# Performance work log

Hardware: AMD Instinct MI355X
Metric: run time of the kernel (lower is better)

## Reference

```python
import jax, jax.numpy as jnp
import numpy as np


def setup_inputs() -> dict:
    key = jax.random.key(0)
    k1, k2, k3, k4 = jax.random.split(key, 4)
    B, Cin, Cout, K, Wd, H, Wsp = 16, 256, 256, 3, 256, 64, 64
    fan_in = Cin * K * K
    return {
        "x": jax.random.normal(k1, (B, Cin, H, Wsp), dtype=jnp.float32),
        "w": jax.random.normal(k2, (B, Wd), dtype=jnp.float32),
        "conv_weight": jax.random.normal(k3, (Cout, Cin, K, K), dtype=jnp.float32) * 0.05,
        "style_w": jax.random.normal(k4, (Cin, Wd), dtype=jnp.float32) * 0.05,
        "style_b": jnp.zeros((Cin,), dtype=jnp.float32),
        "scale": jnp.asarray(1.0 / np.sqrt(fan_in), dtype=jnp.float32),
    }


def reference(x, w, conv_weight, style_w, style_b, scale):
    # x: [B, Cin, H, W]; w: [B, Wd]; conv_weight: [Cout, Cin, K, K]
    B, Cin, H, Wsp = x.shape
    Cout, _, K, _ = conv_weight.shape
    # style modulation: s = Linear(w) -> [B, 1, Cin, 1, 1]
    s = (w @ style_w.T + style_b).reshape(B, 1, Cin, 1, 1)
    # modulate + demodulate per-sample weights: [B, Cout, Cin, K, K]
    wt = (conv_weight * scale)[None] * s
    demod = jax.lax.rsqrt(jnp.sum(wt * wt, axis=(2, 3, 4), keepdims=True) + 1e-8)
    wt = (wt * demod).reshape(B * Cout, Cin, K, K)
    # grouped conv emulation: input [1, B*Cin, H, W], groups=B
    xr = x.reshape(1, B * Cin, H, Wsp)
    pad = 1
    out = jax.lax.conv_general_dilated(
        xr, wt,
        window_strides=(1, 1),
        padding=[(pad, pad), (pad, pad)],
        dimension_numbers=("NCHW", "OIHW", "NCHW"),
        feature_group_count=B,
    )
    return out.reshape(B, Cout, out.shape[2], out.shape[3])
```

## Files before the change

kernel.cpp:

```cpp
#include <hip/hip_runtime.h>
#include <hip/hip_bf16.h>

#define BB   16
#define CIN  256
#define COUT 256
#define WD   256
#define HH   64
#define WWS  64
#define NSP  4096
#define KW   9

typedef __attribute__((ext_vector_type(8))) short short8;
typedef __attribute__((ext_vector_type(4))) float f32x4;
typedef unsigned short ushort_t;
typedef unsigned int uint_t;

#define S_BYTES (BB*CIN*4)
#define WT_OFF (S_BYTES)
#define WT_BYTES (BB*9*COUT*CIN*2)
#define X_OFF (WT_OFF + WT_BYTES)
#define X_BYTES (BB*NSP*CIN*2)
#define ZP_OFF (X_OFF + X_BYTES)
#define ZP_BYTES 4096
#define WS_NEEDED ((size_t)(ZP_OFF + ZP_BYTES))

#define WAITVM0 asm volatile("s_waitcnt vmcnt(0)" ::: "memory")
#define WAITVM3 asm volatile("s_waitcnt vmcnt(3)" ::: "memory")

__device__ inline ushort_t f2bf(float f) {
    __hip_bfloat16 h = __float2bfloat16(f);
    return __builtin_bit_cast(ushort_t, h);
}

__device__ inline void gload_lds16(const ushort_t* g, ushort_t* l) {
    __builtin_amdgcn_global_load_lds(
        (const __attribute__((address_space(1))) void*)g,
        (__attribute__((address_space(3))) void*)l, 16, 0, 0);
}

__global__ __launch_bounds__(256)
void zero_kernel(float* __restrict__ zp) {
    ((float4*)zp)[threadIdx.x] = make_float4(0.f, 0.f, 0.f, 0.f);
}

__global__ __launch_bounds__(256)
void style_kernel(const float* __restrict__ w,
                  const float* __restrict__ style_w,
                  const float* __restrict__ style_b,
                  float* __restrict__ s) {
    const int b  = blockIdx.x;
    const int ci = threadIdx.x;
    __shared__ float wsh[WD];
    wsh[ci] = w[b * WD + ci];
    __syncthreads();
    const float* row = style_w + ci * WD;
    float acc = style_b[ci];
    #pragma unroll 4
    for (int k = 0; k < WD; ++k) acc += wsh[k] * row[k];
    s[b * CIN + ci] = acc;
}

__global__ __launch_bounds__(256)
void wt_kernel(const float* __restrict__ cw, const float* __restrict__ s,
               const float* __restrict__ scale_p, ushort_t* __restrict__ wt) {
    const int co = blockIdx.x, b = blockIdx.y, ci = threadIdx.x;
    const float sv = s[b * CIN + ci] * scale_p[0];
    const float* cp = cw + ((size_t)co * CIN + ci) * KW;
    float v[9];
    float ss = 0.f;
    #pragma unroll
    for (int t = 0; t < 9; ++t) { v[t] = cp[t] * sv; ss += v[t] * v[t]; }
    #pragma unroll
    for (int off = 32; off > 0; off >>= 1) ss += __shfl_down(ss, off);
    __shared__ float red[4];
    if ((ci & 63) == 0) red[ci >> 6] = ss;
    __syncthreads();
    const float dm = rsqrtf(red[0] + red[1] + red[2] + red[3] + 1e-8f);
    #pragma unroll
    for (int t = 0; t < 9; ++t)
        wt[((size_t)(b * 9 + t) * COUT + co) * CIN + ci] = f2bf(v[t] * dm);
}

__global__ __launch_bounds__(256)
void xpose_kernel(const float* __restrict__ x, ushort_t* __restrict__ xo) {
    const int spt = blockIdx.x;
    const int cit = blockIdx.y;
    const int b   = blockIdx.z;
    const int t   = threadIdx.x;
    __shared__ ushort_t tile[64 * 68];
    const int sp0 = spt * 64, ci0 = cit * 64;
    {
        const int spq = t & 15, cil = t >> 4;
        #pragma unroll
        for (int i = 0; i < 4; ++i) {
            const int ci = cil + i * 16;
            const float4 v = *(const float4*)(x + ((size_t)(b * CIN + ci0 + ci)) * NSP + sp0 + spq * 4);
            tile[(spq * 4 + 0) * 68 + ci] = f2bf(v.x);
            tile[(spq * 4 + 1) * 68 + ci] = f2bf(v.y);
            tile[(spq * 4 + 2) * 68 + ci] = f2bf(v.z);
            tile[(spq * 4 + 3) * 68 + ci] = f2bf(v.w);
        }
    }
    __syncthreads();
    {
        const int g4 = t & 15, sp = t >> 4;
        #pragma unroll
        for (int i = 0; i < 4; ++i) {
            const int spp = sp + i * 16;
            uint2 v = *(const uint2*)&tile[spp * 68 + g4 * 4];
            *(uint2*)(xo + ((size_t)(b * NSP + sp0 + spp)) * CIN + ci0 + g4 * 4) = v;
        }
    }
}

__global__ __launch_bounds__(512, 2)
void conv_mfma_kernel(const ushort_t* __restrict__ wt,
                      const ushort_t* __restrict__ xo,
                      const ushort_t* __restrict__ zp,
                      float* __restrict__ out) {
    const int wg    = blockIdx.x;
    const int b     = wg & 15;
    const int ntile = wg >> 4;
    const int y0    = ntile * 4;

    const int tid  = threadIdx.x;
    const int lane = tid & 63;
    const int w    = tid >> 6;
    const int wm   = w >> 1;
    const int wn   = w & 1;
    const int l15  = lane & 15;
    const int lg   = lane >> 4;

    __shared__ __align__(16) ushort_t lds_a[2 * 3 * 256 * 32];
    __shared__ __align__(16) ushort_t lds_x[2 * 6 * 66 * 32];

    const int keyW  = ((lane >> 2) ^ (lane >> 4)) & 3;
    const uint_t srcq8 = (uint_t)(((lane & 3) ^ keyW) * 8);

    const uint_t wtb    = (uint_t)b * 9u * COUT * CIN;
    const uint_t a_src0 = (uint_t)(tid >> 2) * 256u + srcq8;
    const int    tid8   = tid * 8;

    const int hi  = tid >> 8;
    const int col = (tid >> 2) & 63;
    const int xdb = hi * 2112 + (col + 1) * 32 + (lane & 3) * 8;
    const ushort_t* px[3];
    #pragma unroll
    for (int j = 0; j < 3; ++j) {
        const int y = y0 - 1 + hi + 2 * j;
        px[j] = (y >= 0 && y < HH)
              ? (xo + (uint_t)b * (NSP * CIN) + (uint_t)(y * WWS + col) * CIN + srcq8)
              : (zp + lane * 8);
    }

    const int slotA8 = (lg ^ ((l15 ^ (l15 >> 2)) & 3)) * 8;
    int slotB8[3];
    #pragma unroll
    for (int kx = 0; kx < 3; ++kx) {
        int c2 = l15 + kx - 1;
        if (c2 < 0) c2 = 0;
        slotB8[kx] = (lg ^ ((c2 ^ (c2 >> 2)) & 3)) * 8;
    }
    const int abase = (wm * 64 + l15) * 32 + slotA8;

    f32x4 acc[4][8];
    #pragma unroll
    for (int mi = 0; mi < 4; ++mi)
        #pragma unroll
        for (int ni = 0; ni < 8; ++ni) acc[mi][ni] = (f32x4){0.f, 0.f, 0.f, 0.f};

    if (tid < 96) {
        const int cell = tid >> 2, qq = tid & 3;
        const int buf = cell / 12, cr = cell % 12;
        const int r = cr >> 1, hc = (cr & 1) * 65;
        *(uint4*)&lds_x[buf * 12672 + r * 2112 + hc * 32 + qq * 8] =
            make_uint4(0, 0, 0, 0);
    }
    asm volatile("s_waitcnt lgkmcnt(0)" ::: "memory");
    __builtin_amdgcn_sched_barrier(0);

    #define ISSUE_A(TB, CHN, DSTSEL)                                           \
    {   ushort_t* adst_ = lds_a + (DSTSEL) * 24576;                            \
        _Pragma("unroll")                                                      \
        for (int i_ = 0; i_ < 6; ++i_)                                         \
            gload_lds16(wt + (wtb + (uint_t)((TB) + (i_ >> 1)) * 65536u        \
                              + (uint_t)(CHN) * 32u + a_src0                   \
                              + (uint_t)(i_ & 1) * 32768u),                    \
                        adst_ + tid8 + i_ * 4096);                             \
    }
    #define ISSUE_X(CS, DSTSEL)                                                \
    {   ushort_t* xdst_ = lds_x + (DSTSEL) * 12672;                            \
        _Pragma("unroll")                                                      \
        for (int j_ = 0; j_ < 3; ++j_)                                         \
            gload_lds16(px[j_] + (CS) * 32, xdst_ + xdb + j_ * 4224);          \
    }
    #define READF(AF, BF, TG)                                                  \
    {   _Pragma("unroll")                                                      \
        for (int mi_ = 0; mi_ < 4; ++mi_)                                      \
            AF[mi_] = *(const short8*)(ab + (TG) * 8192 + mi_ * 512);          \
        _Pragma("unroll")                                                      \
        for (int ni_ = 0; ni_ < 8; ++ni_)                                      \
            BF[ni_] = *(const short8*)(xb + (xrow + (ni_ >> 2)) * 2112         \
                        + ((ni_ & 3) * 16 + l15 + (TG)) * 32 + slotB8[TG]);    \
    }
    #define MFMAC(AF, BF)                                                      \
    {   __builtin_amdgcn_s_setprio(1);                                         \
        _Pragma("unroll")                                                      \
        for (int mi_ = 0; mi_ < 4; ++mi_)                                      \
            _Pragma("unroll")                                                  \
            for (int ni_ = 0; ni_ < 8; ++ni_)                                  \
                acc[mi_][ni_] = __builtin_amdgcn_mfma_f32_16x16x32_bf16(       \
                    BF[ni_], AF[mi_], acc[mi_][ni_], 0, 0, 0);                 \
        __builtin_amdgcn_s_setprio(0);                                         \
    }

    ISSUE_X(0, 0);
    ISSUE_A(0, 0, 0);

    #pragma unroll 1
    for (int chunk = 0; chunk < 8; ++chunk) {
        #pragma unroll
        for (int gph = 0; gph < 3; ++gph) {
            if (gph == 2 && chunk != 7) { WAITVM3; } else { WAITVM0; }
            __builtin_amdgcn_sched_barrier(0);
            __builtin_amdgcn_s_barrier();
            __builtin_amdgcn_sched_barrier(0);

            const int Gpar = (chunk ^ gph) & 1;
            if (!(chunk == 7 && gph == 2)) {
                const int tb2 = ((gph + 1) % 3) * 3;
                const int chn = chunk + (gph == 2 ? 1 : 0);
                ISSUE_A(tb2, chn, Gpar ^ 1);
            }
            if (gph == 1 && chunk < 7) ISSUE_X(chunk + 1, (chunk + 1) & 1);

            const ushort_t* ab = lds_a + Gpar * 24576 + abase;
            const ushort_t* xb = lds_x + (chunk & 1) * 12672;
            const int xrow = wn * 2 + gph;

            short8 af0[4], bf0[8], af1[4], bf1[8];
            READF(af0, bf0, 0);
            READF(af1, bf1, 1);
            MFMAC(af0, bf0);
            READF(af0, bf0, 2);
            MFMAC(af1, bf1);
            MFMAC(af0, bf0);
        }
    }

    #pragma unroll
    for (int mi = 0; mi < 4; ++mi) {
        const int co = wm * 64 + mi * 16 + l15;
        float* ob = out + ((long)(b * COUT + co)) * NSP
                  + ntile * 256 + wn * 128 + lg * 4;
        #pragma unroll
        for (int ni = 0; ni < 8; ++ni)
            *(f32x4*)(ob + ni * 16) = acc[mi][ni];
    }
    #undef ISSUE_A
    #undef ISSUE_X
    #undef READF
    #undef MFMAC
}

__global__ __launch_bounds__(256)
void modconv_kernel(const float* __restrict__ x,
                    const float* __restrict__ cw,
                    const float* __restrict__ s,
                    const float* __restrict__ scale_p,
                    float* __restrict__ out) {
    const int tile = blockIdx.x;
    const int co   = blockIdx.y;
    const int b    = blockIdx.z;
    const int tid  = threadIdx.x;
    const float scale = scale_p[0];

    __shared__ float s_wt[CIN * KW];
    __shared__ float s_x[18 * 66];
    __shared__ float red[4];

    const float* cwb = cw + (size_t)co * CIN * KW;
    const float* sb  = s + b * CIN;
    float sumsq = 0.f;
    for (int i = tid; i < CIN * KW; i += 256) {
        float v = cwb[i] * scale * sb[i / KW];
        s_wt[i] = v;
        sumsq += v * v;
    }
    #pragma unroll
    for (int off = 32; off > 0; off >>= 1) sumsq += __shfl_down(sumsq, off);
    if ((tid & 63) == 0) red[tid >> 6] = sumsq;
    __syncthreads();
    const float demod = rsqrtf(red[0] + red[1] + red[2] + red[3] + 1e-8f);
    for (int i = tid; i < CIN * KW; i += 256) s_wt[i] *= demod;

    const int tx = tid & 63;
    const int tr = tid >> 6;
    const int y0 = tile * 16;
    float acc[4] = {0.f, 0.f, 0.f, 0.f};

    for (int ci = 0; ci < CIN; ++ci) {
        __syncthreads();
        const float* xb = x + ((size_t)(b * CIN + ci)) * (HH * WWS);
        for (int idx = tid; idx < 18 * 66; idx += 256) {
            const int r = idx / 66, c = idx % 66;
            const int yg = y0 - 1 + r, xg = c - 1;
            float v = 0.f;
            if (yg >= 0 && yg < HH && xg >= 0 && xg < WWS) v = xb[yg * WWS + xg];
            s_x[idx] = v;
        }
        __syncthreads();
        const float* wr = s_wt + ci * KW;
        const float w0 = wr[0], w1 = wr[1], w2 = wr[2];
        const float w3 = wr[3], w4 = wr[4], w5 = wr[5];
        const float w6 = wr[6], w7 = wr[7], w8 = wr[8];
        const int rbase = tr * 4;
        float xv[6][3];
        #pragma unroll
        for (int j = 0; j < 6; ++j)
            #pragma unroll
            for (int k = 0; k < 3; ++k) xv[j][k] = s_x[(rbase + j) * 66 + tx + k];
        #pragma unroll
        for (int i = 0; i < 4; ++i)
            acc[i] += w0 * xv[i][0] + w1 * xv[i][1] + w2 * xv[i][2]
                    + w3 * xv[i+1][0] + w4 * xv[i+1][1] + w5 * xv[i+1][2]
                    + w6 * xv[i+2][0] + w7 * xv[i+2][1] + w8 * xv[i+2][2];
    }
    float* ob = out + (((size_t)(b * COUT + co)) * HH + y0) * WWS + tx;
    #pragma unroll
    for (int i = 0; i < 4; ++i) ob[(tr * 4 + i) * WWS] = acc[i];
}

extern "C" void kernel_launch(void* const* d_in, const int* in_sizes, int n_in,
                              void* d_out, int out_size, void* d_ws, size_t ws_size,
                              hipStream_t stream) {
    const float* x       = (const float*)d_in[0];
    const float* w       = (const float*)d_in[1];
    const float* cw      = (const float*)d_in[2];
    const float* style_w = (const float*)d_in[3];
    const float* style_b = (const float*)d_in[4];
    const float* scale_p = (const float*)d_in[5];
    float*       out     = (float*)d_out;

    float*    s    = (float*)d_ws;
    ushort_t* wswt = (ushort_t*)((char*)d_ws + WT_OFF);
    ushort_t* wsx  = (ushort_t*)((char*)d_ws + X_OFF);
    float*    zp   = (float*)((char*)d_ws + ZP_OFF);

    style_kernel<<<dim3(BB), 256, 0, stream>>>(w, style_w, style_b, s);

    if (ws_size >= WS_NEEDED) {
        zero_kernel<<<dim3(1), 256, 0, stream>>>(zp);
        wt_kernel<<<dim3(COUT, BB), 256, 0, stream>>>(cw, s, scale_p, wswt);
        xpose_kernel<<<dim3(64, 4, BB), 256, 0, stream>>>(x, wsx);
        conv_mfma_kernel<<<dim3(256), 512, 0, stream>>>(wswt, wsx,
                                                        (const ushort_t*)zp, out);
    } else {
        modconv_kernel<<<dim3(4, COUT, BB), 256, 0, stream>>>(x, cw, s, scale_p, out);
    }
}
```

Measured before the change: 123.6 us.

## Restructure conv MFMA main loop into per-wave tap pipeline with register double-buffering

Rewrites the conv MFMA kernel so each wave loads its own slice of the weight tile into a 3-slot LDS ring and loops tap by tap. Fragments are prefetched into double-buffered registers, so most of the per-tap block barriers go away and only one barrier per chunk remains. The zero kernel is folded into wt_kernel to save a launch, and the transpose kernel's stores are widened to 16 bytes. The cost is a more intricate vmcnt-based synchronisation scheme, where a wrong wait count could cause races, plus higher register pressure.

```diff
diff --git a/kernel.cpp b/kernel.cpp
--- a/kernel.cpp
+++ b/kernel.cpp
@@ -24,8 +24,8 @@
 #define ZP_BYTES 4096
 #define WS_NEEDED ((size_t)(ZP_OFF + ZP_BYTES))
 
-#define WAITVM0 asm volatile("s_waitcnt vmcnt(0)" ::: "memory")
-#define WAITVM3 asm volatile("s_waitcnt vmcnt(3)" ::: "memory")
+#define WAITVM4 asm volatile("s_waitcnt vmcnt(4)" ::: "memory")
+#define WAITVM7 asm volatile("s_waitcnt vmcnt(7)" ::: "memory")
 
 __device__ inline ushort_t f2bf(float f) {
     __hip_bfloat16 h = __float2bfloat16(f);
@@ -36,11 +36,6 @@
     __builtin_amdgcn_global_load_lds(
         (const __attribute__((address_space(1))) void*)g,
         (__attribute__((address_space(3))) void*)l, 16, 0, 0);
-}
-
-__global__ __launch_bounds__(256)
-void zero_kernel(float* __restrict__ zp) {
-    ((float4*)zp)[threadIdx.x] = make_float4(0.f, 0.f, 0.f, 0.f);
 }
 
 __global__ __launch_bounds__(256)
@@ -62,8 +57,11 @@
 
 __global__ __launch_bounds__(256)
 void wt_kernel(const float* __restrict__ cw, const float* __restrict__ s,
-               const float* __restrict__ scale_p, ushort_t* __restrict__ wt) {
+               const float* __restrict__ scale_p, ushort_t* __restrict__ wt,
+               float* __restrict__ zp) {
     const int co = blockIdx.x, b = blockIdx.y, ci = threadIdx.x;
+    if (co == 0 && b == 0)
+        ((float4*)zp)[ci] = make_float4(0.f, 0.f, 0.f, 0.f);
     const float sv = s[b * CIN + ci] * scale_p[0];
     const float* cp = cw + ((size_t)co * CIN + ci) * KW;
     float v[9];
@@ -87,7 +85,7 @@
     const int cit = blockIdx.y;
     const int b   = blockIdx.z;
     const int t   = threadIdx.x;
-    __shared__ ushort_t tile[64 * 68];
+    __shared__ ushort_t tile[64 * 72];
     const int sp0 = spt * 64, ci0 = cit * 64;
     {
         const int spq = t & 15, cil = t >> 4;
@@ -95,20 +93,20 @@
         for (int i = 0; i < 4; ++i) {
             const int ci = cil + i * 16;
             const float4 v = *(const float4*)(x + ((size_t)(b * CIN + ci0 + ci)) * NSP + sp0 + spq * 4);
-            tile[(spq * 4 + 0) * 68 + ci] = f2bf(v.x);
-            tile[(spq * 4 + 1) * 68 + ci] = f2bf(v.y);
-            tile[(spq * 4 + 2) * 68 + ci] = f2bf(v.z);
-            tile[(spq * 4 + 3) * 68 + ci] = f2bf(v.w);
+            tile[(spq * 4 + 0) * 72 + ci] = f2bf(v.x);
+            tile[(spq * 4 + 1) * 72 + ci] = f2bf(v.y);
+            tile[(spq * 4 + 2) * 72 + ci] = f2bf(v.z);
+            tile[(spq * 4 + 3) * 72 + ci] = f2bf(v.w);
         }
     }
     __syncthreads();
     {
-        const int g4 = t & 15, sp = t >> 4;
-        #pragma unroll
-        for (int i = 0; i < 4; ++i) {
-            const int spp = sp + i * 16;
-            uint2 v = *(const uint2*)&tile[spp * 68 + g4 * 4];
-            *(uint2*)(xo + ((size_t)(b * NSP + sp0 + spp)) * CIN + ci0 + g4 * 4) = v;
+        const int g8 = t & 7, sp = t >> 3;
+        #pragma unroll
+        for (int i = 0; i < 2; ++i) {
+            const int spp = sp + i * 32;
+            uint4 v = *(const uint4*)&tile[spp * 72 + g8 * 8];
+            *(uint4*)(xo + ((size_t)(b * NSP + sp0 + spp)) * CIN + ci0 + g8 * 8) = v;
         }
     }
 }
@@ -119,7 +117,7 @@
                       const ushort_t* __restrict__ zp,
                       float* __restrict__ out) {
     const int wg    = blockIdx.x;
-    const int b     = wg & 15;
+    const int b     = (wg & 7) | (((wg >> 3) & 1) << 3);
     const int ntile = wg >> 4;
     const int y0    = ntile * 4;
 
@@ -128,29 +126,33 @@
     const int w    = tid >> 6;
     const int wm   = w >> 1;
     const int wn   = w & 1;
+    const int wn2  = wn * 2;
     const int l15  = lane & 15;
     const int lg   = lane >> 4;
-
-    __shared__ __align__(16) ushort_t lds_a[2 * 3 * 256 * 32];
+    const int lane8 = lane * 8;
+
+    __shared__ __align__(16) ushort_t lds_a[8 * 3 * 2048];
     __shared__ __align__(16) ushort_t lds_x[2 * 6 * 66 * 32];
 
-    const int keyW  = ((lane >> 2) ^ (lane >> 4)) & 3;
-    const uint_t srcq8 = (uint_t)(((lane & 3) ^ keyW) * 8);
-
-    const uint_t wtb    = (uint_t)b * 9u * COUT * CIN;
-    const uint_t a_src0 = (uint_t)(tid >> 2) * 256u + srcq8;
-    const int    tid8   = tid * 8;
-
-    const int hi  = tid >> 8;
-    const int col = (tid >> 2) & 63;
-    const int xdb = hi * 2112 + (col + 1) * 32 + (lane & 3) * 8;
+    const uint_t srcq8 = (uint_t)(((lane & 3) ^ (((lane >> 2) ^ (lane >> 4)) & 3)) * 8);
+
+    const ushort_t* pa = wt + (size_t)b * (9 * COUT * CIN)
+                       + (uint_t)(wm * 64 + (lane >> 2)) * CIN + srcq8;
+    const int awbase = w * 6144;
+
     const ushort_t* px[3];
+    int xdst_off[3];
     #pragma unroll
     for (int j = 0; j < 3; ++j) {
-        const int y = y0 - 1 + hi + 2 * j;
-        px[j] = (y >= 0 && y < HH)
-              ? (xo + (uint_t)b * (NSP * CIN) + (uint_t)(y * WWS + col) * CIN + srcq8)
-              : (zp + lane * 8);
+        const int cell = w * 3 + j;
+        const int r    = cell >> 2;
+        const int cg   = cell & 3;
+        const int col  = cg * 16 + (lane >> 2);
+        const int y    = y0 - 1 + r;
+        const bool val = (y >= 0 && y < HH);
+        px[j] = val ? (xo + (size_t)b * (NSP * CIN) + (uint_t)(y * WWS + col) * CIN + srcq8)
+                    : (zp + lane8);
+        xdst_off[j] = r * 2112 + (cg * 16 + 1) * 32 + lane8;
     }
 
     const int slotA8 = (lg ^ ((l15 ^ (l15 >> 2)) & 3)) * 8;
@@ -161,13 +163,15 @@
         if (c2 < 0) c2 = 0;
         slotB8[kx] = (lg ^ ((c2 ^ (c2 >> 2)) & 3)) * 8;
     }
-    const int abase = (wm * 64 + l15) * 32 + slotA8;
+    const int ardbase = l15 * 32 + slotA8;
 
     f32x4 acc[4][8];
     #pragma unroll
     for (int mi = 0; mi < 4; ++mi)
         #pragma unroll
         for (int ni = 0; ni < 8; ++ni) acc[mi][ni] = (f32x4){0.f, 0.f, 0.f, 0.f};
+
+    short8 af[2][4], bf[2][8];
 
     if (tid < 96) {
         const int cell = tid >> 2, qq = tid & 3;
@@ -176,91 +180,122 @@
         *(uint4*)&lds_x[buf * 12672 + r * 2112 + hc * 32 + qq * 8] =
             make_uint4(0, 0, 0, 0);
     }
+
+    #pragma unroll
+    for (int j = 0; j < 3; ++j)
+        gload_lds16(px[j], lds_x + xdst_off[j]);
+    #pragma unroll
+    for (int i = 0; i < 4; ++i)
+        gload_lds16(pa + i * 4096, lds_a + awbase + i * 512 + lane8);
+    #pragma unroll
+    for (int i = 0; i < 4; ++i)
+        gload_lds16(pa + 65536 + i * 4096, lds_a + awbase + 2048 + i * 512 + lane8);
+
+    WAITVM4;
     asm volatile("s_waitcnt lgkmcnt(0)" ::: "memory");
     __builtin_amdgcn_sched_barrier(0);
-
-    #define ISSUE_A(TB, CHN, DSTSEL)                                           \
-    {   ushort_t* adst_ = lds_a + (DSTSEL) * 24576;                            \
+    __builtin_amdgcn_s_barrier();
+
+    {
+        const ushort_t* ar = lds_a + awbase + ardbase;
+        #pragma unroll
+        for (int mi = 0; mi < 4; ++mi) af[0][mi] = *(const short8*)(ar + mi * 512);
+        #pragma unroll
+        for (int ni = 0; ni < 8; ++ni)
+            bf[0][ni] = *(const short8*)(lds_x + (wn2 + (ni >> 2)) * 2112
+                          + ((ni & 3) * 16 + l15) * 32 + slotB8[0]);
+    }
+
+    #define TAP(t, CP, cvar)                                                   \
+    {                                                                          \
+        constexpr int P_ = ((CP) + (t)) & 1;                                   \
+        constexpr int Q_ = P_ ^ 1;                                             \
+                         \
+        {                                                                      \
+            constexpr int tp2 = ((t) + 2) % 9;                                 \
+            constexpr int bA  = ((t) + 2) % 3;                                 \
+            const int ch2 = ((cvar) + (((t) + 2) / 9)) & 7;                    \
+            const uint_t aoff = (uint_t)tp2 * 65536u + (uint_t)ch2 * 32u;      \
+            ushort_t* ad = lds_a + awbase + bA * 2048 + lane8;                 \
+            _Pragma("unroll")                                                  \
+            for (int i_ = 0; i_ < 4; ++i_)                                     \
+                gload_lds16(pa + aoff + i_ * 4096, ad + i_ * 512);             \
+        }                                                                      \
+        if ((t) == 4) {                        \
+            const int cs = ((cvar) + 1) & 7;                                   \
+            ushort_t* xd = lds_x + ((CP) ^ 1) * 12672;                         \
+            _Pragma("unroll")                                                  \
+            for (int j_ = 0; j_ < 3; ++j_)                                     \
+                gload_lds16(px[j_] + cs * 32, xd + xdst_off[j_]);              \
+        }                                                                      \
+                \
+        if ((t) == 4 || (t) == 5) { WAITVM7; } else { WAITVM4; }               \
+        __builtin_amdgcn_sched_barrier(0);                                     \
+                      \
+        {                                                                      \
+            constexpr int bA1 = ((t) + 1) % 3;                                 \
+            const ushort_t* ar = lds_a + awbase + bA1 * 2048 + ardbase;        \
+            _Pragma("unroll")                                                  \
+            for (int mi_ = 0; mi_ < 4; ++mi_)                                  \
+                af[Q_][mi_] = *(const short8*)(ar + mi_ * 512);                \
+        }                                                                      \
+        if ((t) < 8) {                                                         \
+            constexpr int t1_ = (t) + 1;                                       \
+            constexpr int ky_ = t1_ / 3, kx_ = t1_ % 3;                        \
+            const ushort_t* xr = lds_x + (CP) * 12672;                         \
+            _Pragma("unroll")                                                  \
+            for (int ni_ = 0; ni_ < 8; ++ni_)                                  \
+                bf[Q_][ni_] = *(const short8*)(xr                              \
+                    + (wn2 + (ni_ >> 2) + ky_) * 2112                          \
+                    + ((ni_ & 3) * 16 + l15 + kx_) * 32 + slotB8[kx_]);        \
+        }                                                                      \
+        __builtin_amdgcn_s_setprio(1);                                         \
         _Pragma("unroll")                                                      \
-        for (int i_ = 0; i_ < 6; ++i_)                                         \
-            gload_lds16(wt + (wtb + (uint_t)((TB) + (i_ >> 1)) * 65536u        \
-                              + (uint_t)(CHN) * 32u + a_src0                   \
-                              + (uint_t)(i_ & 1) * 32768u),                    \
-                        adst_ + tid8 + i_ * 4096);                             \
-    }
-    #define ISSUE_X(CS, DSTSEL)                                                \
-    {   ushort_t* xdst_ = lds_x + (DSTSEL) * 12672;                            \
-        _Pragma("unroll")                                                      \
-        for (int j_ = 0; j_ < 3; ++j_)                                         \
-            gload_lds16(px[j_] + (CS) * 32, xdst_ + xdb + j_ * 4224);          \
-    }
-    #define READF(AF, BF, TG)                                                  \
-    {   _Pragma("unroll")                                                      \
         for (int mi_ = 0; mi_ < 4; ++mi_)                                      \
-            AF[mi_] = *(const short8*)(ab + (TG) * 8192 + mi_ * 512);          \
+            _Pragma("unroll")                                                  \
+            for (int ni_ = 0; ni_ < 8; ++ni_)                                  \
+                acc[mi_][ni_] = __builtin_amdgcn_mfma_f32_16x16x32_bf16(       \
+                    bf[P_][ni_], af[P_][mi_], acc[mi_][ni_], 0, 0, 0);         \
+        __builtin_amdgcn_s_setprio(0);                                         \
+        __builtin_amdgcn_sched_barrier(0);                                     \
+    }
+
+    #define CHUNK_TAIL(CP, cvar)                                               \
+    {                                                                          \
+        __builtin_amdgcn_s_barrier();    \
+        constexpr int Q_ = ((CP) + 9) & 1;                                     \
+        const ushort_t* xr = lds_x + ((CP) ^ 1) * 12672;                       \
         _Pragma("unroll")                                                      \
         for (int ni_ = 0; ni_ < 8; ++ni_)                                      \
-            BF[ni_] = *(const short8*)(xb + (xrow + (ni_ >> 2)) * 2112         \
-                        + ((ni_ & 3) * 16 + l15 + (TG)) * 32 + slotB8[TG]);    \
-    }
-    #define MFMAC(AF, BF)                                                      \
-    {   __builtin_amdgcn_s_setprio(1);                                         \
-        _Pragma("unroll")                                                      \
-        for (int mi_ = 0; mi_ < 4; ++mi_)                                      \
-            _Pragma("unroll")                                                  \
-            for (int ni_ = 0; ni_ < 8; ++ni_)                                  \
-                acc[mi_][ni_] = __builtin_amdgcn_mfma_f32_16x16x32_bf16(       \
-                    BF[ni_], AF[mi_], acc[mi_][ni_], 0, 0, 0);                 \
-        __builtin_amdgcn_s_setprio(0);                                         \
-    }
-
-    ISSUE_X(0, 0);
-    ISSUE_A(0, 0, 0);
+            bf[Q_][ni_] = *(const short8*)(xr + (wn2 + (ni_ >> 2)) * 2112      \
+                + ((ni_ & 3) * 16 + l15) * 32 + slotB8[0]);                    \
+    }
 
     #pragma unroll 1
-    for (int chunk = 0; chunk < 8; ++chunk) {
-        #pragma unroll
-        for (int gph = 0; gph < 3; ++gph) {
-            if (gph == 2 && chunk != 7) { WAITVM3; } else { WAITVM0; }
-            __builtin_amdgcn_sched_barrier(0);
-            __builtin_amdgcn_s_barrier();
-            __builtin_amdgcn_sched_barrier(0);
-
-            const int Gpar = (chunk ^ gph) & 1;
-            if (!(chunk == 7 && gph == 2)) {
-                const int tb2 = ((gph + 1) % 3) * 3;
-                const int chn = chunk + (gph == 2 ? 1 : 0);
-                ISSUE_A(tb2, chn, Gpar ^ 1);
-            }
-            if (gph == 1 && chunk < 7) ISSUE_X(chunk + 1, (chunk + 1) & 1);
-
-            const ushort_t* ab = lds_a + Gpar * 24576 + abase;
-            const ushort_t* xb = lds_x + (chunk & 1) * 12672;
-            const int xrow = wn * 2 + gph;
-
-            short8 af0[4], bf0[8], af1[4], bf1[8];
-            READF(af0, bf0, 0);
-            READF(af1, bf1, 1);
-            MFMAC(af0, bf0);
-            READF(af0, bf0, 2);
-            MFMAC(af1, bf1);
-            MFMAC(af0, bf0);
-        }
-    }
+    for (int c2 = 0; c2 < 4; ++c2) {
+        const int ce = c2 * 2, cd = ce + 1;
+        TAP(0, 0, ce) TAP(1, 0, ce) TAP(2, 0, ce) TAP(3, 0, ce) TAP(4, 0, ce)
+        TAP(5, 0, ce) TAP(6, 0, ce) TAP(7, 0, ce) TAP(8, 0, ce)
+        CHUNK_TAIL(0, ce)
+        TAP(0, 1, cd) TAP(1, 1, cd) TAP(2, 1, cd) TAP(3, 1, cd) TAP(4, 1, cd)
+        TAP(5, 1, cd) TAP(6, 1, cd) TAP(7, 1, cd) TAP(8, 1, cd)
+        CHUNK_TAIL(1, cd)
+    }
+    #undef TAP
+    #undef CHUNK_TAIL
+
+    asm volatile("s_waitcnt vmcnt(0) lgkmcnt(0)" ::: "memory");
+    __builtin_amdgcn_sched_barrier(0);
 
     #pragma unroll
     for (int mi = 0; mi < 4; ++mi) {
         const int co = wm * 64 + mi * 16 + l15;
-        float* ob = out + ((long)(b * COUT + co)) * NSP
+        float* ob = out + ((size_t)(b * COUT + co)) * NSP
                   + ntile * 256 + wn * 128 + lg * 4;
         #pragma unroll
         for (int ni = 0; ni < 8; ++ni)
-            *(f32x4*)(ob + ni * 16) = acc[mi][ni];
-    }
-    #undef ISSUE_A
-    #undef ISSUE_X
-    #undef READF
-    #undef MFMAC
+            *(f32x4*)(ob + (ni >> 2) * 64 + (ni & 3) * 16) = acc[mi][ni];
+    }
 }
 
 __global__ __launch_bounds__(256)
@@ -350,8 +385,7 @@
     style_kernel<<<dim3(BB), 256, 0, stream>>>(w, style_w, style_b, s);
 
     if (ws_size >= WS_NEEDED) {
-        zero_kernel<<<dim3(1), 256, 0, stream>>>(zp);
-        wt_kernel<<<dim3(COUT, BB), 256, 0, stream>>>(cw, s, scale_p, wswt);
+        wt_kernel<<<dim3(COUT, BB), 256, 0, stream>>>(cw, s, scale_p, wswt, zp);
         xpose_kernel<<<dim3(64, 4, BB), 256, 0, stream>>>(x, wsx);
         conv_mfma_kernel<<<dim3(256), 512, 0, stream>>>(wswt, wsx,
                                                         (const ushort_t*)zp, out);
```

New measurement: 112.4 us. 9.0% less time.
